# Performance work log

Hardware: AMD Instinct MI355X
Metric: run time of the kernel (lower is better)

Reference implementation:

```python
import jax, jax.numpy as jnp
import numpy as np

N = 100000   # total nodes across all graphs
E = 1600000  # edges (avg degree 16)
D = 128      # input feature dim
H = 64       # hidden dim
B = 8        # number of graphs
EPS = 1e-5   # BatchNorm eps


def setup_inputs() -> dict:
    key = jax.random.key(0)
    ks = jax.random.split(key, 12)
    x = jax.random.normal(ks[0], (N, D), dtype=jnp.float32)
    edge_index = jax.random.randint(ks[1], (2, E), 0, N, dtype=jnp.int64)
    batch = jnp.sort(jax.random.randint(ks[2], (N,), 0, B, dtype=jnp.int64))
    s1 = 1.0 / np.sqrt(D)
    s2 = 1.0 / np.sqrt(H)
    W1l = jax.random.uniform(ks[3], (D, H), minval=-s1, maxval=s1, dtype=jnp.float32)
    W1r = jax.random.uniform(ks[4], (D, H), minval=-s1, maxval=s1, dtype=jnp.float32)
    b1 = jnp.zeros((H,), jnp.float32)
    gamma1 = jnp.ones((H,), jnp.float32)
    beta1 = jnp.zeros((H,), jnp.float32)
    W2l = jax.random.uniform(ks[5], (H, H), minval=-s2, maxval=s2, dtype=jnp.float32)
    W2r = jax.random.uniform(ks[6], (H, H), minval=-s2, maxval=s2, dtype=jnp.float32)
    b2 = jnp.zeros((H,), jnp.float32)
    return {"x": x, "edge_index": edge_index, "batch": batch,
            "W1l": W1l, "b1": b1, "W1r": W1r, "gamma1": gamma1, "beta1": beta1,
            "W2l": W2l, "b2": b2, "W2r": W2r}


def _seg_mean(vals, idx, num):
    # scatter-mean: sum per segment / count, zero-degree segments give 0 (count clamped)
    s = jax.ops.segment_sum(vals, idx, num_segments=num)
    cnt = jax.ops.segment_sum(jnp.ones((idx.shape[0], 1), vals.dtype), idx, num_segments=num)
    return s / jnp.maximum(cnt, 1.0)


def reference(x, edge_index, batch, W1l, b1, W1r, gamma1, beta1, W2l, b2, W2r):
    src, dst = edge_index[0], edge_index[1]
    # SAGEConv layer 1: mean-aggregate neighbors, lin_l(agg) + lin_r(x)
    agg1 = _seg_mean(x[src], dst, N)            # [N, D]
    h = agg1 @ W1l + b1 + x @ W1r               # [N, H]
    # BatchNorm1d (training-mode batch stats, biased var) then ReLU
    mu = jnp.mean(h, axis=0)
    var = jnp.var(h, axis=0)
    h = (h - mu) * jax.lax.rsqrt(var + EPS) * gamma1 + beta1
    h = jax.nn.relu(h)
    # SAGEConv layer 2 (no norm/act after last layer)
    agg2 = _seg_mean(h[src], dst, N)            # [N, H]
    h2 = agg2 @ W2l + b2 + h @ W2r              # [N, H]
    # per-graph global mean pool -> [B, H]
    return _seg_mean(h2, batch, B)
```

## Files before the change

kernel.cpp:

```cpp
#include <hip/hip_runtime.h>

#define N_NODES 100000
#define E_EDGES 1600000
#define DIM 128
#define HID 64
#define NGRAPH 8
#define EPSBN 1e-5f

#define GSHIFT 9
#define GNODES (1 << GSHIFT)
#define NGROUP ((N_NODES + GNODES - 1) >> GSHIFT)
#define GCAP 10240
#define CHUNK 2048
#define PBLK 256
#define EPT (CHUNK / PBLK)
#define NCHUNK ((E_EDGES + CHUNK - 1) / CHUNK)
#define MM1B ((N_NODES + 63) / 64)
#define GATB 2048

#if __has_builtin(__builtin_amdgcn_cvt_pk_fp8_f32) && \
    __has_builtin(__builtin_amdgcn_cvt_pk_f32_fp8)
#define HW_FP8 1
#else
#define HW_FP8 0
#endif

typedef float floatx2 __attribute__((ext_vector_type(2)));
typedef short bf16x8 __attribute__((ext_vector_type(8)));
typedef float f32x4 __attribute__((ext_vector_type(4)));

__device__ __forceinline__ int colOfPos(int p) {
  return 16 * (p & 3) + (p >> 2);
}

__device__ __forceinline__ unsigned f2bf_pack(float lo, float hi) {
  unsigned ul = __float_as_uint(lo);
  unsigned uh = __float_as_uint(hi);
  ul = (ul + 0x7fffu + ((ul >> 16) & 1u)) >> 16;
  uh = (uh + 0x7fffu + ((uh >> 16) & 1u)) >> 16;
  return (uh << 16) | ul;
}
__device__ __forceinline__ float bflo(unsigned u) {
  return __uint_as_float(u << 16);
}
__device__ __forceinline__ float bfhi(unsigned u) {
  return __uint_as_float(u & 0xffff0000u);
}

#if !HW_FP8
__device__ __forceinline__ unsigned char f32_to_e4m3(float f) {
  unsigned u = __float_as_uint(f);
  unsigned s = (u >> 24) & 0x80u;
  float a = fabsf(f);
  if (a >= 464.f) return (unsigned char)(s | 0x7E);
  if (a < 0.015625f) {
    int m = (int)rintf(a * 512.f);
    if (m >= 8) return (unsigned char)(s | 0x08);
    return (unsigned char)(s | (unsigned)m);
  }
  int e = (int)((u >> 23) & 0xFF) - 127;
  float q = ldexpf(a, -e) * 8.f;
  int m = (int)rintf(q);
  if (m == 16) { m = 8; ++e; }
  if (e > 8) return (unsigned char)(s | 0x7E);
  return (unsigned char)(s | (unsigned)(((e + 7) << 3) | (m - 8)));
}
#endif

__device__ __forceinline__ unsigned pack4_e4m3(float a, float b, float c,
                                               float d) {
#if HW_FP8
  int w = __builtin_amdgcn_cvt_pk_fp8_f32(a, b, 0, false);
  w = __builtin_amdgcn_cvt_pk_fp8_f32(c, d, w, true);
  return (unsigned)w;
#else
  return (unsigned)f32_to_e4m3(a) | ((unsigned)f32_to_e4m3(b) << 8) |
         ((unsigned)f32_to_e4m3(c) << 16) | ((unsigned)f32_to_e4m3(d) << 24);
#endif
}

__global__ __launch_bounds__(64) void wprep_kernel(
    const float* __restrict__ W1l, const float* __restrict__ W1r,
    unsigned* __restrict__ wTbf) {
  int n = blockIdx.x;
  int kp = threadIdx.x;
  const float* Wc = (n < 64) ? (W1l + n) : (W1r + (n - 64));
  float w0 = Wc[(size_t)(2 * kp) * HID];
  float w1 = Wc[(size_t)(2 * kp + 1) * HID];
  wTbf[n * 64 + kp] = f2bf_pack(w0, w1);
}

__global__ __launch_bounds__(PBLK) void part_mm1_kernel(
    const int* __restrict__ src, const int* __restrict__ dst,
    int* __restrict__ gcnt, unsigned* __restrict__ part,
    const float* __restrict__ x, const unsigned* __restrict__ wTbf,
    unsigned char* __restrict__ y1f8, unsigned* __restrict__ y2bf) {
  __shared__ __align__(16) unsigned char smraw[17536];

  if (blockIdx.x < NCHUNK) {
    int* hist = (int*)(smraw);
    int* sc = (int*)(smraw + 1024);
    int* scanoff = (int*)(smraw + 2048);
    int* gbase = (int*)(smraw + 3072);
    unsigned* buf = (unsigned*)(smraw + 4096);
    unsigned char* gid = smraw + 12288;

    int c = blockIdx.x;
    int e0 = c * CHUNK;
    int m = E_EDGES - e0;
    m = m < CHUNK ? m : CHUNK;
    int t = threadIdx.x;

    hist[t] = 0;
    __syncthreads();

    int myg[EPT];
    unsigned mytok[EPT];
    int myrank[EPT];
    #pragma unroll
    for (int q = 0; q < EPT; ++q) {
      int i = t + q * PBLK;
      if (i < m) {
        int d = dst[e0 + i];
        int s = src[e0 + i];
        int g = d >> GSHIFT;
        myg[q] = g;
        mytok[q] = ((unsigned)(d & (GNODES - 1)) << 17) | (unsigned)s;
        myrank[q] = atomicAdd(&hist[g], 1);
      } else {
        myg[q] = -1;
      }
    }
    __syncthreads();

    sc[t] = hist[t];
    if (t < NGROUP && hist[t] > 0) gbase[t] = atomicAdd(&gcnt[t], hist[t]);
    __syncthreads();
    for (int off = 1; off < 256; off <<= 1) {
      int add = (t >= off) ? sc[t - off] : 0;
      __syncthreads();
      sc[t] += add;
      __syncthreads();
    }
    scanoff[t] = sc[t] - hist[t];
    __syncthreads();

    #pragma unroll
    for (int q = 0; q < EPT; ++q) {
      if (myg[q] >= 0) {
        int pos = scanoff[myg[q]] + myrank[q];
        buf[pos] = mytok[q];
        gid[pos] = (unsigned char)myg[q];
      }
    }
    __syncthreads();

    for (int i = t; i < m; i += PBLK) {
      int g = gid[i];
      int addr = gbase[g] + (i - scanoff[g]);
      if (addr < GCAP) part[(size_t)g * GCAP + addr] = buf[i];
    }
  } else {
    short* xs = (short*)smraw;
    int t = threadIdx.x;
    int brow = (blockIdx.x - NCHUNK) * 64;

    for (int i = t; i < 64 * 32; i += PBLK) {
      int r = i >> 5;
      int c4 = (i & 31) << 2;
      int n = brow + r;
      unsigned lo = 0u, hi = 0u;
      if (n < N_NODES) {
        float4 v = *reinterpret_cast<const float4*>(x + (size_t)n * DIM + c4);
        lo = f2bf_pack(v.x, v.y);
        hi = f2bf_pack(v.z, v.w);
      }
      unsigned* dp = (unsigned*)(xs + r * 136 + c4);
      dp[0] = lo;
      dp[1] = hi;
    }
    __syncthreads();

    int lane = t & 63;
    int w = t >> 6;
    int l15 = lane & 15;
    int lg = lane >> 4;

    f32x4 acc[8];
    #pragma unroll
    for (int j = 0; j < 8; ++j) acc[j] = (f32x4){0.f, 0.f, 0.f, 0.f};

    #pragma unroll
    for (int ks = 0; ks < 4; ++ks) {
      int k0 = ks * 32 + lg * 8;
      bf16x8 a = *(const bf16x8*)(xs + (w * 16 + l15) * 136 + k0);
      bf16x8 bfr[8];
      #pragma unroll
      for (int nf = 0; nf < 8; ++nf) {
        const uint4* bp = reinterpret_cast<const uint4*>(
            wTbf + (nf * 16 + l15) * 64 + ks * 16 + lg * 4);
        uint4 bv = *bp;
        bfr[nf] = *(const bf16x8*)&bv;
      }
      #pragma unroll
      for (int nf = 0; nf < 8; ++nf)
        acc[nf] =
            __builtin_amdgcn_mfma_f32_16x16x32_bf16(a, bfr[nf], acc[nf], 0,
                                                    0, 0);
    }

    #pragma unroll
    for (int rg = 0; rg < 4; ++rg) {
      int r = w * 16 + lg * 4 + rg;
      int n = brow + r;
      if (n < N_NODES) {
        unsigned p1 = pack4_e4m3(acc[0][rg], acc[1][rg], acc[2][rg],
                                 acc[3][rg]);
        *reinterpret_cast<unsigned*>(y1f8 + (size_t)n * HID + l15 * 4) = p1;
        uint2 p2;
        p2.x = f2bf_pack(acc[4][rg], acc[5][rg]);
        p2.y = f2bf_pack(acc[6][rg], acc[7][rg]);
        *reinterpret_cast<uint2*>(y2bf + (size_t)n * (HID / 2) + l15 * 2) =
            p2;
      }
    }
  }
}

__global__ __launch_bounds__(512) void groupcsr_kernel(
    const int* __restrict__ gcnt, const unsigned* __restrict__ part,
    const int* __restrict__ batch, int* __restrict__ rowptr,
    int* __restrict__ csr, unsigned* __restrict__ tok2) {
  __shared__ int hist[GNODES];
  __shared__ int excl[GNODES];
  __shared__ int degl[GNODES];
  __shared__ int batl[GNODES];
  __shared__ int sc2[256];
  int g = blockIdx.x;
  int t = threadIdx.x;

  if (t < 256) sc2[t] = (t < NGROUP) ? min(gcnt[t], GCAP) : 0;
  __syncthreads();
  for (int off = 1; off < 256; off <<= 1) {
    int add = (t < 256 && t >= off) ? sc2[t - off] : 0;
    __syncthreads();
    if (t < 256) sc2[t] += add;
    __syncthreads();
  }
  int gbase = (g > 0) ? sc2[g - 1] : 0;

  hist[t] = 0;
  {
    int n = (g << GSHIFT) + t;
    batl[t] = (n < N_NODES) ? batch[n] : 0;
  }
  __syncthreads();

  int cnt = min(gcnt[g], GCAP);
  const unsigned* ga = part + (size_t)g * GCAP;
  for (int i = t; i < cnt; i += 512) atomicAdd(&hist[ga[i] >> 17], 1);
  __syncthreads();

  int orig = hist[t];
  degl[t] = orig;
  for (int off = 1; off < GNODES; off <<= 1) {
    int add = (t >= off) ? hist[t - off] : 0;
    __syncthreads();
    hist[t] += add;
    __syncthreads();
  }
  excl[t] = hist[t] - orig;
  __syncthreads();

  int n = (g << GSHIFT) + t;
  if (n <= N_NODES) rowptr[n] = gbase + excl[t];
  if (g == 0 && t == 0) rowptr[0] = 0;
  __syncthreads();

  for (int i = t; i < cnt; i += 512) {
    unsigned p = ga[i];
    int dloc = (int)(p >> 17);
    int pos = gbase + atomicAdd(&excl[dloc], 1);
    unsigned s = p & 0x1FFFFu;
    csr[pos] = (int)s;
    unsigned dg = (unsigned)degl[dloc];
    if (dg > 1023u) dg = 1023u;
    tok2[pos] = (dg << 20) | ((unsigned)batl[dloc] << 17) | s;
  }
}

__global__ __launch_bounds__(PBLK) void part2_gather_kernel(
    const unsigned* __restrict__ tok2, int* __restrict__ gcnt2,
    unsigned* __restrict__ part2, const uint2* __restrict__ yf8,
    const int* __restrict__ csr, const int* __restrict__ rowptr,
    const unsigned* __restrict__ otherbf, const float* __restrict__ bias,
    unsigned* __restrict__ outCbf, float* __restrict__ stats) {
  __shared__ int hist[256];
  __shared__ int sc[256];
  __shared__ int scanoff[256];
  __shared__ int gbase[256];
  __shared__ unsigned buf[CHUNK];
  __shared__ unsigned char gid[CHUNK];
  __shared__ float ss[HID];
  __shared__ float sq[HID];

  if (blockIdx.x < NCHUNK) {
    int c = blockIdx.x;
    int e0 = c * CHUNK;
    int m = E_EDGES - e0;
    m = m < CHUNK ? m : CHUNK;
    int t = threadIdx.x;

    hist[t] = 0;
    __syncthreads();

    int myg[EPT];
    unsigned mytok[EPT];
    int myrank[EPT];
    #pragma unroll
    for (int q = 0; q < EPT; ++q) {
      int i = t + q * PBLK;
      if (i < m) {
        unsigned p = tok2[e0 + i];
        int g = (int)((p & 0x1FFFFu) >> GSHIFT);
        myg[q] = g;
        mytok[q] = p;
        myrank[q] = atomicAdd(&hist[g], 1);
      } else {
        myg[q] = -1;
      }
    }
    __syncthreads();

    sc[t] = hist[t];
    if (t < NGROUP && hist[t] > 0) gbase[t] = atomicAdd(&gcnt2[t], hist[t]);
    __syncthreads();
    for (int off = 1; off < 256; off <<= 1) {
      int add = (t >= off) ? sc[t - off] : 0;
      __syncthreads();
      sc[t] += add;
      __syncthreads();
    }
    scanoff[t] = sc[t] - hist[t];
    __syncthreads();

    #pragma unroll
    for (int q = 0; q < EPT; ++q) {
      if (myg[q] >= 0) {
        int pos = scanoff[myg[q]] + myrank[q];
        buf[pos] = mytok[q];
        gid[pos] = (unsigned char)myg[q];
      }
    }
    __syncthreads();

    for (int i = t; i < m; i += PBLK) {
      int g = gid[i];
      int addr = gbase[g] + (i - scanoff[g]);
      if (addr < GCAP) part2[(size_t)g * GCAP + addr] = buf[i];
    }
  } else {
#if !HW_FP8
    __shared__ float tbl[256];
    {
      int t = threadIdx.x;
      if (t < 256) {
        int e = (t >> 3) & 15;
        int m = t & 7;
        float v = e ? ldexpf((float)(8 + m), e - 10) : ldexpf((float)m, -9);
        tbl[t] = (t & 0x80) ? -v : v;
      }
    }
    __syncthreads();
#endif
    int lane = threadIdx.x & 63;
    int oct = lane >> 3;
    int lo = lane & 7;
    int gbid = blockIdx.x - NCHUNK;
    int wid = (gbid * PBLK + (int)threadIdx.x) >> 6;
    const int nw = (GATB * PBLK) >> 6;

    float bj[8];
    #pragma unroll
    for (int k = 0; k < 8; ++k) bj[k] = bias[colOfPos(lo * 8 + k)];

    float ls[8], lq[8];
    #pragma unroll
    for (int k = 0; k < 8; ++k) { ls[k] = 0.f; lq[k] = 0.f; }

    for (int nb = wid * 8; nb < N_NODES; nb += nw * 8) {
      int n = nb + oct;
      bool valid = n < N_NODES;
      int start = valid ? rowptr[n] : 0;
      int end = valid ? rowptr[n + 1] : 0;

      float acc[8];
      #pragma unroll
      for (int k = 0; k < 8; ++k) acc[k] = 0.f;

      for (int bse = start; bse < end; bse += 8) {
        int m = end - bse;
        m = m < 8 ? m : 8;
        int e = bse + lo;
        int s = (e < end) ? csr[e] : 0;
        uint2 vv[8];
        #pragma unroll
        for (int i = 0; i < 8; ++i) {
          int si = __shfl(s, i, 8);
          vv[i] = yf8[(size_t)si * 8 + lo];
        }
        #pragma unroll
        for (int i = 0; i < 8; ++i) {
          if (i < m) {
#if HW_FP8
            floatx2 p0 = __builtin_amdgcn_cvt_pk_f32_fp8((int)vv[i].x, false);
            floatx2 p1 = __builtin_amdgcn_cvt_pk_f32_fp8((int)vv[i].x, true);
            floatx2 p2 = __builtin_amdgcn_cvt_pk_f32_fp8((int)vv[i].y, false);
            floatx2 p3 = __builtin_amdgcn_cvt_pk_f32_fp8((int)vv[i].y, true);
            acc[0] += p0[0];
            acc[1] += p0[1];
            acc[2] += p1[0];
            acc[3] += p1[1];
            acc[4] += p2[0];
            acc[5] += p2[1];
            acc[6] += p3[0];
            acc[7] += p3[1];
#else
            acc[0] += tbl[vv[i].x & 255u];
            acc[1] += tbl[(vv[i].x >> 8) & 255u];
            acc[2] += tbl[(vv[i].x >> 16) & 255u];
            acc[3] += tbl[vv[i].x >> 24];
            acc[4] += tbl[vv[i].y & 255u];
            acc[5] += tbl[(vv[i].y >> 8) & 255u];
            acc[6] += tbl[(vv[i].y >> 16) & 255u];
            acc[7] += tbl[vv[i].y >> 24];
#endif
          }
        }
      }

      if (valid) {
        int deg = end - start;
        float inv = 1.f / (float)(deg > 1 ? deg : 1);
        uint4 ov = *reinterpret_cast<const uint4*>(otherbf +
                                                   (size_t)n * (HID / 2) +
                                                   lo * 4);
        float v[8];
        v[0] = fmaf(acc[0], inv, bj[0]) + bflo(ov.x);
        v[1] = fmaf(acc[1], inv, bj[1]) + bfhi(ov.x);
        v[2] = fmaf(acc[2], inv, bj[2]) + bflo(ov.y);
        v[3] = fmaf(acc[3], inv, bj[3]) + bfhi(ov.y);
        v[4] = fmaf(acc[4], inv, bj[4]) + bflo(ov.z);
        v[5] = fmaf(acc[5], inv, bj[5]) + bfhi(ov.z);
        v[6] = fmaf(acc[6], inv, bj[6]) + bflo(ov.w);
        v[7] = fmaf(acc[7], inv, bj[7]) + bfhi(ov.w);
        uint4 cw4;
        cw4.x = f2bf_pack(v[0], v[1]);
        cw4.y = f2bf_pack(v[2], v[3]);
        cw4.z = f2bf_pack(v[4], v[5]);
        cw4.w = f2bf_pack(v[6], v[7]);
        *reinterpret_cast<uint4*>(outCbf + (size_t)n * (HID / 2) + lo * 4) =
            cw4;
        #pragma unroll
        for (int k = 0; k < 8; ++k) {
          ls[k] += v[k];
          lq[k] = fmaf(v[k], v[k], lq[k]);
        }
      }
    }

    int t = threadIdx.x;
    if (t < HID) { ss[t] = 0.f; sq[t] = 0.f; }
    __syncthreads();
    #pragma unroll
    for (int k = 0; k < 8; ++k) {
      atomicAdd(&ss[lo * 8 + k], ls[k]);
      atomicAdd(&sq[lo * 8 + k], lq[k]);
    }
    __syncthreads();
    if (t < HID) {
      unsafeAtomicAdd(&stats[t], ss[t]);
      unsafeAtomicAdd(&stats[HID + t], sq[t]);
    }
  }
}

__global__ __launch_bounds__(256) void chsum_kernel(
    const int* __restrict__ gcnt2, const unsigned* __restrict__ part2,
    const unsigned* __restrict__ Cbf, const float* __restrict__ stats,
    const float* __restrict__ gamma, const float* __restrict__ beta,
    const int* __restrict__ batch, float* __restrict__ S1g,
    float* __restrict__ S2g) {
  __shared__ float c[GNODES * NGRAPH];
  __shared__ float r1[HID * NGRAPH];
  __shared__ float r2[HID * NGRAPH];
  int g = blockIdx.x;
  int t = threadIdx.x;

  for (int i = t; i < GNODES * NGRAPH; i += 256) c[i] = 0.f;
  for (int i = t; i < HID * NGRAPH; i += 256) { r1[i] = 0.f; r2[i] = 0.f; }
  __syncthreads();

  int cnt = min(gcnt2[g], GCAP);
  const unsigned* ga = part2 + (size_t)g * GCAP;
  for (int i = t; i < cnt; i += 256) {
    unsigned p = ga[i];
    int sl = (int)(p & (GNODES - 1));
    int b = (int)((p >> 17) & 7u);
    int deg = (int)((p >> 20) & 0x3FFu);
    float w = 1.f / (float)(deg > 1 ? deg : 1);
    atomicAdd(&c[sl * NGRAPH + b], w);
  }
  __syncthreads();

  int lane = t & 63;
  int wv = t >> 6;
  int cl = colOfPos(lane);

  float inv_n = 1.0f / (float)N_NODES;
  float mu = stats[lane] * inv_n;
  float var = stats[HID + lane] * inv_n - mu * mu;
  float scl = gamma[cl] * rsqrtf(var + EPSBN);
  float shf = beta[cl] - mu * scl;

  float s1[NGRAPH], s2[NGRAPH];
  #pragma unroll
  for (int b = 0; b < NGRAPH; ++b) { s1[b] = 0.f; s2[b] = 0.f; }

  int nend = N_NODES - (g << GSHIFT);
  nend = nend < GNODES ? nend : GNODES;
  for (int nl = wv; nl < nend; nl += 4) {
    int n = (g << GSHIFT) + nl;
    unsigned u = Cbf[(size_t)n * (HID / 2) + (lane >> 1)];
    float hr = (lane & 1) ? bfhi(u) : bflo(u);
    float h = fmaf(hr, scl, shf);
    h = h > 0.f ? h : 0.f;
    int bn = batch[n];
    #pragma unroll
    for (int b = 0; b < NGRAPH; ++b) {
      float cb = c[nl * NGRAPH + b];
      s1[b] = fmaf(cb, h, s1[b]);
      s2[b] += (b == bn) ? h : 0.f;
    }
  }

  #pragma unroll
  for (int b = 0; b < NGRAPH; ++b) {
    atomicAdd(&r1[b * HID + lane], s1[b]);
    atomicAdd(&r2[b * HID + lane], s2[b]);
  }
  __syncthreads();
  for (int i = t; i < HID * NGRAPH; i += 256) {
    unsafeAtomicAdd(&S1g[i], r1[i]);
    unsafeAtomicAdd(&S2g[i], r2[i]);
  }
}

__device__ __forceinline__ int lbound(const int* __restrict__ a, int key) {
  int lo = 0, hi = N_NODES;
  while (lo < hi) {
    int mid = (lo + hi) >> 1;
    if (a[mid] < key) lo = mid + 1; else hi = mid;
  }
  return lo;
}

__global__ __launch_bounds__(512) void finale_kernel(
    const float* __restrict__ S1g, const float* __restrict__ S2g,
    const int* __restrict__ batch, const float* __restrict__ W2l,
    const float* __restrict__ W2r, const float* __restrict__ b2,
    float* __restrict__ out) {
  int t = threadIdx.x;
  int b = t >> 6;
  int oc = t & 63;
  int V = lbound(batch, b + 1) - lbound(batch, b);
  float acc = 0.f;
  for (int l = 0; l < HID; ++l) {
    int k = colOfPos(l);
    acc = fmaf(S1g[b * HID + l], W2l[k * HID + oc], acc);
    acc = fmaf(S2g[b * HID + l], W2r[k * HID + oc], acc);
  }
  out[t] = (V > 0) ? (acc / (float)V + b2[oc]) : 0.f;
}

extern "C" void kernel_launch(void* const* d_in, const int* in_sizes, int n_in,
                              void* d_out, int out_size, void* d_ws,
                              size_t ws_size, hipStream_t stream) {
  const float* x      = (const float*)d_in[0];
  const int*   ei     = (const int*)d_in[1];
  const int*   batch  = (const int*)d_in[2];
  const float* W1l    = (const float*)d_in[3];
  const float* b1     = (const float*)d_in[4];
  const float* W1r    = (const float*)d_in[5];
  const float* gamma1 = (const float*)d_in[6];
  const float* beta1  = (const float*)d_in[7];
  const float* W2l    = (const float*)d_in[8];
  const float* b2     = (const float*)d_in[9];
  const float* W2r    = (const float*)d_in[10];

  const int* src = ei;
  const int* dst = ei + E_EDGES;

  float* ws = (float*)d_ws;
  size_t off = 0;
  unsigned char* Af8 = (unsigned char*)(ws + off);
  off += (size_t)N_NODES * HID / 4;
  unsigned* Bbf = (unsigned*)(ws + off);
  off += (size_t)N_NODES * (HID / 2);
  unsigned* Cbf = (unsigned*)(ws + off);
  off += (size_t)N_NODES * (HID / 2);
  int* gcnt     = (int*)(ws + off); off += 256;
  int* gcnt2    = (int*)(ws + off); off += 256;
  float* stats  = ws + off; off += 2 * HID;
  float* S1g    = ws + off; off += NGRAPH * HID;
  float* S2g    = ws + off; off += NGRAPH * HID;
  size_t zero_elems = 256 + 256 + 2 * HID + 2 * NGRAPH * HID;
  unsigned* wTbf = (unsigned*)(ws + off); off += 128 * 64;
  int* rowptr   = (int*)(ws + off); off += N_NODES + 1;
  int* csr      = (int*)(ws + off); off += E_EDGES;
  unsigned* tok2 = (unsigned*)(ws + off); off += E_EDGES;
  unsigned* part = (unsigned*)(ws + off); off += (size_t)NGROUP * GCAP;

  hipMemsetAsync(gcnt, 0, zero_elems * sizeof(float), stream);

  wprep_kernel<<<128, 64, 0, stream>>>(W1l, W1r, wTbf);

  part_mm1_kernel<<<NCHUNK + MM1B, PBLK, 0, stream>>>(
      src, dst, gcnt, part, x, wTbf, Af8, Bbf);

  groupcsr_kernel<<<NGROUP, 512, 0, stream>>>(gcnt, part, batch, rowptr, csr,
                                              tok2);

  part2_gather_kernel<<<NCHUNK + GATB, PBLK, 0, stream>>>(
      tok2, gcnt2, part, (const uint2*)Af8, csr, rowptr, Bbf, b1, Cbf, stats);

  chsum_kernel<<<NGROUP, 256, 0, stream>>>(gcnt2, part, Cbf, stats, gamma1,
                                           beta1, batch, S1g, S2g);

  finale_kernel<<<1, 512, 0, stream>>>(S1g, S2g, batch, W2l, W2r, b2,
                                       (float*)d_out);
}
```

Before: 254.9 us.

## Regroup kernels: fuse weight prep into partition, fuse mm1 with group CSR build

Weight transposition to bf16 now runs as extra blocks of the edge-partition kernel, and the first dense matmul runs as extra blocks of the group-CSR kernel, which removes one kernel launch and moves the matmul off the partition pass. The matmul stages the transposed weights in shared memory, uses 512-thread blocks with only half the threads issuing MFMA, and allocates 52KB of LDS, which may lower occupancy. The chsum kernel goes from 256 to 512 threads per block. The matmul now depends on the partition kernel finishing, which changes the overlap between the partition and matmul work.

```diff
diff --git a/kernel.cpp b/kernel.cpp
--- a/kernel.cpp
+++ b/kernel.cpp
@@ -17,6 +17,7 @@
 #define NCHUNK ((E_EDGES + CHUNK - 1) / CHUNK)
 #define MM1B ((N_NODES + 63) / 64)
 #define GATB 2048
+#define WPREPB 32
 
 #if __has_builtin(__builtin_amdgcn_cvt_pk_fp8_f32) && \
     __has_builtin(__builtin_amdgcn_cvt_pk_f32_fp8)
@@ -79,32 +80,19 @@
 #endif
 }
 
-__global__ __launch_bounds__(64) void wprep_kernel(
+__global__ __launch_bounds__(PBLK) void part_wprep_kernel(
+    const int* __restrict__ src, const int* __restrict__ dst,
+    int* __restrict__ gcnt, unsigned* __restrict__ part,
     const float* __restrict__ W1l, const float* __restrict__ W1r,
     unsigned* __restrict__ wTbf) {
-  int n = blockIdx.x;
-  int kp = threadIdx.x;
-  const float* Wc = (n < 64) ? (W1l + n) : (W1r + (n - 64));
-  float w0 = Wc[(size_t)(2 * kp) * HID];
-  float w1 = Wc[(size_t)(2 * kp + 1) * HID];
-  wTbf[n * 64 + kp] = f2bf_pack(w0, w1);
-}
-
-__global__ __launch_bounds__(PBLK) void part_mm1_kernel(
-    const int* __restrict__ src, const int* __restrict__ dst,
-    int* __restrict__ gcnt, unsigned* __restrict__ part,
-    const float* __restrict__ x, const unsigned* __restrict__ wTbf,
-    unsigned char* __restrict__ y1f8, unsigned* __restrict__ y2bf) {
-  __shared__ __align__(16) unsigned char smraw[17536];
+  __shared__ int hist[256];
+  __shared__ int sc[256];
+  __shared__ int scanoff[256];
+  __shared__ int gbase[256];
+  __shared__ unsigned buf[CHUNK];
+  __shared__ unsigned char gid[CHUNK];
 
   if (blockIdx.x < NCHUNK) {
-    int* hist = (int*)(smraw);
-    int* sc = (int*)(smraw + 1024);
-    int* scanoff = (int*)(smraw + 2048);
-    int* gbase = (int*)(smraw + 3072);
-    unsigned* buf = (unsigned*)(smraw + 4096);
-    unsigned char* gid = smraw + 12288;
-
     int c = blockIdx.x;
     int e0 = c * CHUNK;
     int m = E_EDGES - e0;
@@ -161,11 +149,33 @@
       if (addr < GCAP) part[(size_t)g * GCAP + addr] = buf[i];
     }
   } else {
+    int i = (blockIdx.x - NCHUNK) * PBLK + threadIdx.x;
+    if (i < 128 * 64) {
+      int n = i >> 6;
+      int kp = i & 63;
+      const float* Wc = (n < 64) ? (W1l + n) : (W1r + (n - 64));
+      float w0 = Wc[(size_t)(2 * kp) * HID];
+      float w1 = Wc[(size_t)(2 * kp + 1) * HID];
+      wTbf[n * 64 + kp] = f2bf_pack(w0, w1);
+    }
+  }
+}
+
+__global__ __launch_bounds__(512) void mm1_gcsr_kernel(
+    const float* __restrict__ x, const unsigned* __restrict__ wTbf,
+    unsigned char* __restrict__ y1f8, unsigned* __restrict__ y2bf,
+    const int* __restrict__ gcnt, const unsigned* __restrict__ part,
+    const int* __restrict__ batch, int* __restrict__ rowptr,
+    int* __restrict__ csr, unsigned* __restrict__ tok2) {
+  __shared__ __align__(16) unsigned char smraw[52224];
+
+  if (blockIdx.x < MM1B) {
     short* xs = (short*)smraw;
+    short* wts = (short*)(smraw + 17408);
     int t = threadIdx.x;
-    int brow = (blockIdx.x - NCHUNK) * 64;
-
-    for (int i = t; i < 64 * 32; i += PBLK) {
+    int brow = blockIdx.x * 64;
+
+    for (int i = t; i < 64 * 32; i += 512) {
       int r = i >> 5;
       int c4 = (i & 31) << 2;
       int n = brow + r;
@@ -179,113 +189,108 @@
       dp[0] = lo;
       dp[1] = hi;
     }
-    __syncthreads();
-
-    int lane = t & 63;
-    int w = t >> 6;
-    int l15 = lane & 15;
-    int lg = lane >> 4;
-
-    f32x4 acc[8];
-    #pragma unroll
-    for (int j = 0; j < 8; ++j) acc[j] = (f32x4){0.f, 0.f, 0.f, 0.f};
-
-    #pragma unroll
-    for (int ks = 0; ks < 4; ++ks) {
-      int k0 = ks * 32 + lg * 8;
-      bf16x8 a = *(const bf16x8*)(xs + (w * 16 + l15) * 136 + k0);
-      bf16x8 bfr[8];
+    for (int i = t; i < 128 * 64; i += 512) {
+      int nn = i >> 6;
+      int kp = i & 63;
+      *(unsigned*)(wts + nn * 136 + kp * 2) = wTbf[i];
+    }
+    __syncthreads();
+
+    if (t < 256) {
+      int lane = t & 63;
+      int w = t >> 6;
+      int l15 = lane & 15;
+      int lg = lane >> 4;
+
+      f32x4 acc[8];
       #pragma unroll
-      for (int nf = 0; nf < 8; ++nf) {
-        const uint4* bp = reinterpret_cast<const uint4*>(
-            wTbf + (nf * 16 + l15) * 64 + ks * 16 + lg * 4);
-        uint4 bv = *bp;
-        bfr[nf] = *(const bf16x8*)&bv;
-      }
+      for (int j = 0; j < 8; ++j) acc[j] = (f32x4){0.f, 0.f, 0.f, 0.f};
+
       #pragma unroll
-      for (int nf = 0; nf < 8; ++nf)
-        acc[nf] =
-            __builtin_amdgcn_mfma_f32_16x16x32_bf16(a, bfr[nf], acc[nf], 0,
-                                                    0, 0);
-    }
-
-    #pragma unroll
-    for (int rg = 0; rg < 4; ++rg) {
-      int r = w * 16 + lg * 4 + rg;
-      int n = brow + r;
-      if (n < N_NODES) {
-        unsigned p1 = pack4_e4m3(acc[0][rg], acc[1][rg], acc[2][rg],
-                                 acc[3][rg]);
-        *reinterpret_cast<unsigned*>(y1f8 + (size_t)n * HID + l15 * 4) = p1;
-        uint2 p2;
-        p2.x = f2bf_pack(acc[4][rg], acc[5][rg]);
-        p2.y = f2bf_pack(acc[6][rg], acc[7][rg]);
-        *reinterpret_cast<uint2*>(y2bf + (size_t)n * (HID / 2) + l15 * 2) =
-            p2;
-      }
-    }
-  }
-}
-
-__global__ __launch_bounds__(512) void groupcsr_kernel(
-    const int* __restrict__ gcnt, const unsigned* __restrict__ part,
-    const int* __restrict__ batch, int* __restrict__ rowptr,
-    int* __restrict__ csr, unsigned* __restrict__ tok2) {
-  __shared__ int hist[GNODES];
-  __shared__ int excl[GNODES];
-  __shared__ int degl[GNODES];
-  __shared__ int batl[GNODES];
-  __shared__ int sc2[256];
-  int g = blockIdx.x;
-  int t = threadIdx.x;
-
-  if (t < 256) sc2[t] = (t < NGROUP) ? min(gcnt[t], GCAP) : 0;
-  __syncthreads();
-  for (int off = 1; off < 256; off <<= 1) {
-    int add = (t < 256 && t >= off) ? sc2[t - off] : 0;
-    __syncthreads();
-    if (t < 256) sc2[t] += add;
-    __syncthreads();
-  }
-  int gbase = (g > 0) ? sc2[g - 1] : 0;
-
-  hist[t] = 0;
-  {
+      for (int ks = 0; ks < 4; ++ks) {
+        int k0 = ks * 32 + lg * 8;
+        bf16x8 a = *(const bf16x8*)(xs + (w * 16 + l15) * 136 + k0);
+        #pragma unroll
+        for (int nf = 0; nf < 8; ++nf) {
+          bf16x8 b = *(const bf16x8*)(wts + (nf * 16 + l15) * 136 + k0);
+          acc[nf] =
+              __builtin_amdgcn_mfma_f32_16x16x32_bf16(a, b, acc[nf], 0, 0, 0);
+        }
+      }
+
+      #pragma unroll
+      for (int rg = 0; rg < 4; ++rg) {
+        int r = w * 16 + lg * 4 + rg;
+        int n = brow + r;
+        if (n < N_NODES) {
+          unsigned p1 = pack4_e4m3(acc[0][rg], acc[1][rg], acc[2][rg],
+                                   acc[3][rg]);
+          *reinterpret_cast<unsigned*>(y1f8 + (size_t)n * HID + l15 * 4) = p1;
+          uint2 p2;
+          p2.x = f2bf_pack(acc[4][rg], acc[5][rg]);
+          p2.y = f2bf_pack(acc[6][rg], acc[7][rg]);
+          *reinterpret_cast<uint2*>(y2bf + (size_t)n * (HID / 2) + l15 * 2) =
+              p2;
+        }
+      }
+    }
+  } else {
+    int* hist = (int*)smraw;
+    int* excl = (int*)(smraw + 2048);
+    int* degl = (int*)(smraw + 4096);
+    int* batl = (int*)(smraw + 6144);
+    int* sc2 = (int*)(smraw + 8192);
+    int g = blockIdx.x - MM1B;
+    int t = threadIdx.x;
+
+    if (t < 256) sc2[t] = (t < NGROUP) ? min(gcnt[t], GCAP) : 0;
+    __syncthreads();
+    for (int off = 1; off < 256; off <<= 1) {
+      int add = (t < 256 && t >= off) ? sc2[t - off] : 0;
+      __syncthreads();
+      if (t < 256) sc2[t] += add;
+      __syncthreads();
+    }
+    int gbase = (g > 0) ? sc2[g - 1] : 0;
+
+    hist[t] = 0;
+    {
+      int n = (g << GSHIFT) + t;
+      batl[t] = (n < N_NODES) ? batch[n] : 0;
+    }
+    __syncthreads();
+
+    int cnt = min(gcnt[g], GCAP);
+    const unsigned* ga = part + (size_t)g * GCAP;
+    for (int i = t; i < cnt; i += 512) atomicAdd(&hist[ga[i] >> 17], 1);
+    __syncthreads();
+
+    int orig = hist[t];
+    degl[t] = orig;
+    for (int off = 1; off < GNODES; off <<= 1) {
+      int add = (t >= off) ? hist[t - off] : 0;
+      __syncthreads();
+      hist[t] += add;
+      __syncthreads();
+    }
+    excl[t] = hist[t] - orig;
+    __syncthreads();
+
     int n = (g << GSHIFT) + t;
-    batl[t] = (n < N_NODES) ? batch[n] : 0;
-  }
-  __syncthreads();
-
-  int cnt = min(gcnt[g], GCAP);
-  const unsigned* ga = part + (size_t)g * GCAP;
-  for (int i = t; i < cnt; i += 512) atomicAdd(&hist[ga[i] >> 17], 1);
-  __syncthreads();
-
-  int orig = hist[t];
-  degl[t] = orig;
-  for (int off = 1; off < GNODES; off <<= 1) {
-    int add = (t >= off) ? hist[t - off] : 0;
-    __syncthreads();
-    hist[t] += add;
-    __syncthreads();
-  }
-  excl[t] = hist[t] - orig;
-  __syncthreads();
-
-  int n = (g << GSHIFT) + t;
-  if (n <= N_NODES) rowptr[n] = gbase + excl[t];
-  if (g == 0 && t == 0) rowptr[0] = 0;
-  __syncthreads();
-
-  for (int i = t; i < cnt; i += 512) {
-    unsigned p = ga[i];
-    int dloc = (int)(p >> 17);
-    int pos = gbase + atomicAdd(&excl[dloc], 1);
-    unsigned s = p & 0x1FFFFu;
-    csr[pos] = (int)s;
-    unsigned dg = (unsigned)degl[dloc];
-    if (dg > 1023u) dg = 1023u;
-    tok2[pos] = (dg << 20) | ((unsigned)batl[dloc] << 17) | s;
+    if (n <= N_NODES) rowptr[n] = gbase + excl[t];
+    if (g == 0 && t == 0) rowptr[0] = 0;
+    __syncthreads();
+
+    for (int i = t; i < cnt; i += 512) {
+      unsigned p = ga[i];
+      int dloc = (int)(p >> 17);
+      int pos = gbase + atomicAdd(&excl[dloc], 1);
+      unsigned s = p & 0x1FFFFu;
+      csr[pos] = (int)s;
+      unsigned dg = (unsigned)degl[dloc];
+      if (dg > 1023u) dg = 1023u;
+      tok2[pos] = (dg << 20) | ((unsigned)batl[dloc] << 17) | s;
+    }
   }
 }
 
@@ -485,7 +490,7 @@
   }
 }
 
-__global__ __launch_bounds__(256) void chsum_kernel(
+__global__ __launch_bounds__(512) void chsum_kernel(
     const int* __restrict__ gcnt2, const unsigned* __restrict__ part2,
     const unsigned* __restrict__ Cbf, const float* __restrict__ stats,
     const float* __restrict__ gamma, const float* __restrict__ beta,
@@ -497,13 +502,13 @@
   int g = blockIdx.x;
   int t = threadIdx.x;
 
-  for (int i = t; i < GNODES * NGRAPH; i += 256) c[i] = 0.f;
-  for (int i = t; i < HID * NGRAPH; i += 256) { r1[i] = 0.f; r2[i] = 0.f; }
+  for (int i = t; i < GNODES * NGRAPH; i += 512) c[i] = 0.f;
+  for (int i = t; i < HID * NGRAPH; i += 512) { r1[i] = 0.f; r2[i] = 0.f; }
   __syncthreads();
 
   int cnt = min(gcnt2[g], GCAP);
   const unsigned* ga = part2 + (size_t)g * GCAP;
-  for (int i = t; i < cnt; i += 256) {
+  for (int i = t; i < cnt; i += 512) {
     unsigned p = ga[i];
     int sl = (int)(p & (GNODES - 1));
     int b = (int)((p >> 17) & 7u);
@@ -529,7 +534,7 @@
 
   int nend = N_NODES - (g << GSHIFT);
   nend = nend < GNODES ? nend : GNODES;
-  for (int nl = wv; nl < nend; nl += 4) {
+  for (int nl = wv; nl < nend; nl += 8) {
     int n = (g << GSHIFT) + nl;
     unsigned u = Cbf[(size_t)n * (HID / 2) + (lane >> 1)];
     float hr = (lane & 1) ? bfhi(u) : bflo(u);
@@ -550,7 +555,7 @@
     atomicAdd(&r2[b * HID + lane], s2[b]);
   }
   __syncthreads();
-  for (int i = t; i < HID * NGRAPH; i += 256) {
+  for (int i = t; i < HID * NGRAPH; i += 512) {
     unsafeAtomicAdd(&S1g[i], r1[i]);
     unsafeAtomicAdd(&S2g[i], r2[i]);
   }
@@ -623,18 +628,16 @@
 
   hipMemsetAsync(gcnt, 0, zero_elems * sizeof(float), stream);
 
-  wprep_kernel<<<128, 64, 0, stream>>>(W1l, W1r, wTbf);
-
-  part_mm1_kernel<<<NCHUNK + MM1B, PBLK, 0, stream>>>(
-      src, dst, gcnt, part, x, wTbf, Af8, Bbf);
-
-  groupcsr_kernel<<<NGROUP, 512, 0, stream>>>(gcnt, part, batch, rowptr, csr,
-                                              tok2);
+  part_wprep_kernel<<<NCHUNK + WPREPB, PBLK, 0, stream>>>(
+      src, dst, gcnt, part, W1l, W1r, wTbf);
+
+  mm1_gcsr_kernel<<<MM1B + NGROUP, 512, 0, stream>>>(
+      x, wTbf, Af8, Bbf, gcnt, part, batch, rowptr, csr, tok2);
 
   part2_gather_kernel<<<NCHUNK + GATB, PBLK, 0, stream>>>(
       tok2, gcnt2, part, (const uint2*)Af8, csr, rowptr, Bbf, b1, Cbf, stats);
 
-  chsum_kernel<<<NGROUP, 256, 0, stream>>>(gcnt2, part, Cbf, stats, gamma1,
+  chsum_kernel<<<NGROUP, 512, 0, stream>>>(gcnt2, part, Cbf, stats, gamma1,
                                            beta1, batch, S1g, S2g);
 
   finale_kernel<<<1, 512, 0, stream>>>(S1g, S2g, batch, W2l, W2r, b2,
```

After: 225.4 us (median of 2 runs). 11.6% less time.
